# Optimization experiments

Measured on AMD Instinct MI355X. Metric: run time of the kernel, lower is better.

## Reference

```python
import jax, jax.numpy as jnp
import numpy as np

HIDDEN = 2048
N_HEADS = 32
N_KV_HEADS = 8
HEAD_DIM = 64
ROPE_THETA = 500000.0
B, S = 1, 2048


def _rope_tables(seq_len):
    inv_freq = 1.0 / ROPE_THETA ** (jnp.arange(0, HEAD_DIM, 2, dtype=jnp.float32) / HEAD_DIM)
    angles = jnp.arange(seq_len, dtype=jnp.float32)[:, None] * inv_freq[None, :]
    return jnp.cos(angles), jnp.sin(angles)


def _apply_rope(x, cos, sin):
    # x: (B, S, H, D); cos/sin: (S, D//2)
    x1 = x[..., 0::2]
    x2 = x[..., 1::2]
    c = cos[None, :, None, :]
    s = sin[None, :, None, :]
    x1r = x1 * c - x2 * s
    x2r = x1 * s + x2 * c
    return jnp.stack([x1r, x2r], axis=-1).reshape(x.shape)


def setup_inputs() -> dict:
    key = jax.random.key(0)
    ks = jax.random.split(key, 5)
    hidden_states = jax.random.normal(ks[0], (B, S, HIDDEN), dtype=jnp.float32)
    # causal mask, broadcastable over (B, H, S, S)
    attention_mask = jnp.tril(jnp.ones((S, S), dtype=bool))[None, :, :]
    sc = 1.0 / np.sqrt(HIDDEN)
    wq = jax.random.normal(ks[1], (HIDDEN, N_HEADS * HEAD_DIM), dtype=jnp.float32) * sc
    wk = jax.random.normal(ks[2], (HIDDEN, N_KV_HEADS * HEAD_DIM), dtype=jnp.float32) * sc
    wv = jax.random.normal(ks[3], (HIDDEN, N_KV_HEADS * HEAD_DIM), dtype=jnp.float32) * sc
    wo = jax.random.normal(ks[4], (N_HEADS * HEAD_DIM, HIDDEN), dtype=jnp.float32) * sc
    return {"hidden_states": hidden_states, "attention_mask": attention_mask,
            "wq": wq, "wk": wk, "wv": wv, "wo": wo}


def reference(hidden_states, attention_mask, wq, wk, wv, wo):
    b, s, _ = hidden_states.shape
    groups = N_HEADS // N_KV_HEADS
    q = (hidden_states @ wq).reshape(b, s, N_HEADS, HEAD_DIM)
    k = (hidden_states @ wk).reshape(b, s, N_KV_HEADS, HEAD_DIM)
    v = (hidden_states @ wv).reshape(b, s, N_KV_HEADS, HEAD_DIM)
    cos, sin = _rope_tables(s)
    q = _apply_rope(q, cos, sin)
    k = _apply_rope(k, cos, sin)
    k = jnp.repeat(k, groups, axis=2)  # (b, s, H, D)
    v = jnp.repeat(v, groups, axis=2)
    q = q.transpose(0, 2, 1, 3)  # (b, H, s, D)
    k = k.transpose(0, 2, 1, 3)
    v = v.transpose(0, 2, 1, 3)
    scores = jnp.einsum('bhqd,bhkd->bhqk', q, k) / jnp.sqrt(jnp.float32(HEAD_DIM))
    scores = jnp.where(attention_mask[:, None, :, :], scores, -jnp.inf)
    probs = jax.nn.softmax(scores, axis=-1)
    out = jnp.einsum('bhqk,bhkd->bhqd', probs, v)
    out = out.transpose(0, 2, 1, 3).reshape(b, s, N_HEADS * HEAD_DIM)
    return out @ wo
```

## Files before the change

kernel.cpp:

```cpp
#include <hip/hip_runtime.h>

typedef __attribute__((ext_vector_type(8))) short short8;
typedef __attribute__((ext_vector_type(4))) float float4v;

union U4S8 { uint4 u; short8 s; };

__device__ __forceinline__ float bf2f(ushort u) {
    union { uint i; float f; } v; v.i = ((uint)u) << 16; return v.f;
}
__device__ __forceinline__ ushort f2bf(float f) {
    union { uint i; float f; } v; v.f = f;
    return (ushort)((v.i + 0x7FFFu + ((v.i >> 16) & 1u)) >> 16);
}
#if __has_builtin(__builtin_amdgcn_cvt_pk_bf16_f32)
__device__ __forceinline__ uint f2bf_pk(float a, float b) {
    auto r = __builtin_amdgcn_cvt_pk_bf16_f32(a, b);
    return __builtin_bit_cast(uint, r);
}
#else
__device__ __forceinline__ uint f2bf_pk(float a, float b) {
    return (uint)f2bf(a) | ((uint)f2bf(b) << 16);
}
#endif
__device__ __forceinline__ void gld_lds16(const ushort* g, ushort* l) {
    __builtin_amdgcn_global_load_lds((const __attribute__((address_space(1))) unsigned int*)g,
                                     (__attribute__((address_space(3))) unsigned int*)l,
                                     16, 0, 0);
}

__device__ __forceinline__ void tconv_body(const float* in, ushort* out,
                                           int C, int r0, int c0, int tid) {
    __shared__ float t[64][65];
    const int lrow = tid >> 2;
    const int lc   = (tid & 3) * 16;
    const float* ip = in + (size_t)(r0 + lrow) * C + c0 + lc;
#pragma unroll
    for (int i = 0; i < 4; i++) {
        float4 v = *(const float4*)(ip + 4 * i);
        t[lrow][lc + 4 * i + 0] = v.x; t[lrow][lc + 4 * i + 1] = v.y;
        t[lrow][lc + 4 * i + 2] = v.z; t[lrow][lc + 4 * i + 3] = v.w;
    }
    __syncthreads();
    ushort* op = out + (size_t)(c0 + lrow) * 2048 + r0 + lc;
#pragma unroll
    for (int i = 0; i < 8; i++)
        ((uint*)op)[i] = f2bf_pk(t[lc + 2 * i][lrow], t[lc + 2 * i + 1][lrow]);
}

__global__ __launch_bounds__(256) void prep(const float* __restrict__ hidden,
                                            const float* __restrict__ wq,
                                            const float* __restrict__ wk,
                                            const float* __restrict__ wv,
                                            const float* __restrict__ wo,
                                            ushort* __restrict__ hid,
                                            ushort* __restrict__ wT,
                                            ushort* __restrict__ woT) {
    const int bx = blockIdx.x;
    if (bx < 2048) {
        const size_t i = ((size_t)bx * 256 + threadIdx.x) * 8;
        float4 a = *(const float4*)(hidden + i);
        float4 b = *(const float4*)(hidden + i + 4);
        uint4 u;
        u.x = f2bf_pk(a.x, a.y); u.y = f2bf_pk(a.z, a.w);
        u.z = f2bf_pk(b.x, b.y); u.w = f2bf_pk(b.z, b.w);
        *(uint4*)(hid + i) = u;
    } else if (bx < 3584) {
        const int i = bx - 2048;
        const int xx = i % 48, yy = i / 48;
        const float* in; ushort* op; int C, cx;
        if (xx < 32)      { in = wq; op = wT;                        C = 2048; cx = xx; }
        else if (xx < 40) { in = wk; op = wT + (size_t)2048 * 2048;  C = 512;  cx = xx - 32; }
        else              { in = wv; op = wT + (size_t)2560 * 2048;  C = 512;  cx = xx - 40; }
        tconv_body(in, op, C, yy * 64, cx * 64, threadIdx.x);
    } else {
        const int i = bx - 3584;
        tconv_body(wo, woT, 2048, (i >> 5) * 64, (i & 31) * 64, threadIdx.x);
    }
}

template <bool BF16OUT>
__global__ __launch_bounds__(512, 2) void gemm_n128(const ushort* __restrict__ A,
                                                    const ushort* __restrict__ Bt,
                                                    void* __restrict__ Cout,
                                                    int N, int K, int lda, int ropeQKV) {
    __shared__ ushort As[2][2][128 * 32];
    __shared__ ushort Bs[2][2][128 * 32];

    const int tid = threadIdx.x, w = tid >> 6, lane = tid & 63;
    const int lr = lane & 15, quad = lane >> 4;
    const int m0 = blockIdx.x * 128, n0 = blockIdx.y * 128;
    const int wr = w >> 1, wc = w & 1;

    const int srow = lane >> 2;
    const int skb  = (lane & 3) ^ ((srow >> 1) & 3);

    const ushort* Ap = A  + (size_t)(m0 + 16 * w + srow) * lda + skb * 8;
    const ushort* Bp = Bt + (size_t)(n0 + 16 * w + srow) * K + skb * 8;

    float4v acc[2][4];
#pragma unroll
    for (int a = 0; a < 2; a++)
#pragma unroll
        for (int b = 0; b < 4; b++) { acc[a][b][0] = 0.f; acc[a][b][1] = 0.f; acc[a][b][2] = 0.f; acc[a][b][3] = 0.f; }

    const int fsw = (lr >> 1) & 3;
    const int niter = K >> 6;

    gld_lds16(Ap,      &As[0][0][w * 512]);
    gld_lds16(Ap + 32, &As[0][1][w * 512]);
    gld_lds16(Bp,      &Bs[0][0][w * 512]);
    gld_lds16(Bp + 32, &Bs[0][1][w * 512]);

    for (int it = 0; it < niter; it++) {
        const int b = it & 1;

        asm volatile("s_waitcnt vmcnt(0) lgkmcnt(0)\n\ts_barrier" ::: "memory");

        if (it + 1 < niter) {
            const int k1 = (it + 1) << 6;
            gld_lds16(Ap + k1,      &As[1 - b][0][w * 512]);
            gld_lds16(Ap + k1 + 32, &As[1 - b][1][w * 512]);
            gld_lds16(Bp + k1,      &Bs[1 - b][0][w * 512]);
            gld_lds16(Bp + k1 + 32, &Bs[1 - b][1][w * 512]);
        }

#pragma unroll
        for (int kh = 0; kh < 2; kh++) {
            short8 af[2], bf[4];
#pragma unroll
            for (int mt = 0; mt < 2; mt++)
                af[mt] = *(const short8*)&As[b][kh][(wr * 32 + mt * 16 + lr) * 32 + (quad ^ fsw) * 8];
#pragma unroll
            for (int nt = 0; nt < 4; nt++)
                bf[nt] = *(const short8*)&Bs[b][kh][(wc * 64 + nt * 16 + lr) * 32 + (quad ^ fsw) * 8];
#pragma unroll
            for (int mt = 0; mt < 2; mt++)
#pragma unroll
                for (int nt = 0; nt < 4; nt++)
                    acc[mt][nt] = __builtin_amdgcn_mfma_f32_16x16x32_bf16(af[mt], bf[nt], acc[mt][nt], 0, 0, 0);
        }
    }

    const int rbase = m0 + wr * 32 + quad * 4;
    const int cbase = n0 + wc * 64 + lr;
    if (BF16OUT) {
        ushort* Cb = (ushort*)Cout;
        if (ropeQKV && (int)blockIdx.y < 20) {
            const float osc = ((int)blockIdx.y < 16) ? 0.18033688f : 1.0f;
            const float sgn = (lr & 1) ? 1.0f : -1.0f;
#pragma unroll
            for (int nt = 0; nt < 4; nt++) {
                const int col = cbase + nt * 16;
                const int j = (col >> 1) & 31;
                const float inv = __expf(-(float)(2 * j) * (1.0f / 64.0f) * 13.122363377404328f);
#pragma unroll
                for (int mt = 0; mt < 2; mt++)
#pragma unroll
                    for (int r = 0; r < 4; r++) {
                        const int row = rbase + mt * 16 + r;
                        float sn, cs;
                        sincosf((float)row * inv, &sn, &cs);
                        const float mine = acc[mt][nt][r];
                        const float partner = __shfl_xor(mine, 1);
                        Cb[(size_t)row * N + col] = f2bf((mine * cs + sgn * partner * sn) * osc);
                    }
            }
        } else {
#pragma unroll
            for (int mt = 0; mt < 2; mt++)
#pragma unroll
                for (int nt = 0; nt < 4; nt++)
#pragma unroll
                    for (int r = 0; r < 4; r++)
                        Cb[(size_t)(rbase + mt * 16 + r) * N + cbase + nt * 16] = f2bf(acc[mt][nt][r]);
        }
    } else {
        float* Cf = (float*)Cout;
#pragma unroll
        for (int mt = 0; mt < 2; mt++)
#pragma unroll
            for (int nt = 0; nt < 4; nt++)
#pragma unroll
                for (int r = 0; r < 4; r++)
                    Cf[(size_t)(rbase + mt * 16 + r) * N + cbase + nt * 16] = acc[mt][nt][r];
    }
}

__global__ __launch_bounds__(256) void attn_mfma(const ushort* __restrict__ Q,
                                                 const ushort* __restrict__ Kc,
                                                 const ushort* __restrict__ Vc,
                                                 ushort* __restrict__ O0,
                                                 ushort* __restrict__ O1,
                                                 float* __restrict__ L0,
                                                 float* __restrict__ L1) {
    __shared__ ushort Ks[2][64 * 64];
    __shared__ ushort Vt[2][64 * 64];
    __shared__ ushort Ps[4][16 * 64];

    const int tid = threadIdx.x, w = tid >> 6, lane = tid & 63;
    const int lr = lane & 15, quad = lane >> 4;
    const int h = blockIdx.y, g = h >> 2, z = blockIdx.z;

    const int dg = tid & 15;
    const int kl = tid >> 4;
    const int ksub = lane >> 3, dsub = lane & 7;
    ushort* Pw = Ps[w];
    ushort* Op = z ? O1 : O0;
    float*  Lp = z ? L1 : L0;

    const ushort* Vp0 = Vc + g * 64 + dg * 4 + (size_t)3072 * kl;
    const ushort* Kp0 = Kc + g * 64 + ((dsub ^ ksub) * 8) + (size_t)3072 * ksub;

    short8 onesf;
#pragma unroll
    for (int j = 0; j < 8; j++) onesf[j] = (short)0x3F80;

    for (int ti = 0; ti < 2; ti++) {
        const int bx = ti ? 31 - (int)blockIdx.x : (int)blockIdx.x;
        const int nch = (bx >= z) ? ((bx - z) >> 1) + 1 : 0;
        const int last = z + 2 * (nch - 1);

        const ushort* qp = Q + (size_t)(bx * 64 + w * 16 + lr) * 3072 + h * 64 + quad * 8;
        const short8 qf0 = *(const short8*)qp;
        const short8 qf1 = *(const short8*)(qp + 32);

        float4v oacc[4], lacc;
#pragma unroll
        for (int t = 0; t < 4; t++) { oacc[t][0] = 0.f; oacc[t][1] = 0.f; oacc[t][2] = 0.f; oacc[t][3] = 0.f; }
        lacc[0] = 0.f; lacc[1] = 0.f; lacc[2] = 0.f; lacc[3] = 0.f;

        uint2 vv[4];
        if (nch) {
#pragma unroll
            for (int t = 0; t < 4; t++)
                vv[t] = *(const uint2*)(Vp0 + (size_t)(z * 64 + 16 * t) * 3072);
        }
        __syncthreads();
        if (nch) {
#pragma unroll
            for (int i = 0; i < 2; i++) {
                const int rt = 2 * w + i;
                gld_lds16(Kp0 + (size_t)(z * 64 + rt * 8) * 3072, &Ks[0][rt * 512]);
            }
        }

        for (int c = 0; c < nch; c++) {
            const int kb = z + 2 * c;
            const int b = c & 1;
            ushort* bKs = Ks[b];
            ushort* bVt = Vt[b];

#pragma unroll
            for (int i = 0; i < 4; i++) {
                const uint sel = (i & 1) ? 0x07060302u : 0x05040100u;
                uint s0 = (i < 2) ? vv[0].x : vv[0].y;
                uint s1 = (i < 2) ? vv[1].x : vv[1].y;
                uint s2 = (i < 2) ? vv[2].x : vv[2].y;
                uint s3 = (i < 2) ? vv[3].x : vv[3].y;
                uint2 pk;
                pk.x = __builtin_amdgcn_perm(s1, s0, sel);
                pk.y = __builtin_amdgcn_perm(s3, s2, sel);
                *(uint2*)&bVt[(dg * 4 + i) * 64 + (kl ^ ((dg & 3) * 4 + i)) * 4] = pk;
            }

            const int kn = (c + 1 < nch) ? kb + 2 : last;
#pragma unroll
            for (int t = 0; t < 4; t++)
                vv[t] = *(const uint2*)(Vp0 + (size_t)(kn * 64 + 16 * t) * 3072);

            asm volatile("s_waitcnt vmcnt(4) lgkmcnt(0)\n\ts_barrier" ::: "memory");

#pragma unroll
            for (int i = 0; i < 2; i++) {
                const int rt = 2 * w + i;
                gld_lds16(Kp0 + (size_t)(kn * 64 + rt * 8) * 3072, &Ks[1 - b][rt * 512]);
            }

            float4v sacc[4];
#pragma unroll
            for (int t = 0; t < 4; t++) { sacc[t][0] = 0.f; sacc[t][1] = 0.f; sacc[t][2] = 0.f; sacc[t][3] = 0.f; }
#pragma unroll
            for (int t = 0; t < 4; t++) {
                const int krow = t * 16 + lr;
                const int sw = lr & 7;
                short8 kf0 = *(const short8*)&bKs[krow * 64 + ((quad)     ^ sw) * 8];
                short8 kf1 = *(const short8*)&bKs[krow * 64 + ((quad + 4) ^ sw) * 8];
                sacc[t] = __builtin_amdgcn_mfma_f32_16x16x32_bf16(qf0, kf0, sacc[t], 0, 0, 0);
                sacc[t] = __builtin_amdgcn_mfma_f32_16x16x32_bf16(qf1, kf1, sacc[t], 0, 0, 0);
            }

            if (kb == bx) {
#pragma unroll
                for (int r = 0; r < 4; r++) {
                    const int qr = w * 16 + quad * 4 + r;
                    float p0 = exp2f(sacc[0][r]), p1 = exp2f(sacc[1][r]);
                    float p2 = exp2f(sacc[2][r]), p3 = exp2f(sacc[3][r]);
                    if (lr > qr)      p0 = 0.f;
                    if (16 + lr > qr) p1 = 0.f;
                    if (32 + lr > qr) p2 = 0.f;
                    if (48 + lr > qr) p3 = 0.f;
                    const int prow = quad * 4 + r;
                    uint2 pk; pk.x = f2bf_pk(p0, p1); pk.y = f2bf_pk(p2, p3);
                    *(uint2*)&Pw[prow * 64 + (lr ^ prow) * 4] = pk;
                }
            } else {
#pragma unroll
                for (int r = 0; r < 4; r++) {
                    const int prow = quad * 4 + r;
                    uint2 pk;
                    pk.x = f2bf_pk(exp2f(sacc[0][r]), exp2f(sacc[1][r]));
                    pk.y = f2bf_pk(exp2f(sacc[2][r]), exp2f(sacc[3][r]));
                    *(uint2*)&Pw[prow * 64 + (lr ^ prow) * 4] = pk;
                }
            }

#pragma unroll
            for (int ks2 = 0; ks2 < 2; ks2++) {
                const int ub = ks2 * 8 + quad * 2;
                U4S8 pu;
                uint2 plo = *(const uint2*)&Pw[lr * 64 + ((ub)     ^ lr) * 4];
                uint2 phi = *(const uint2*)&Pw[lr * 64 + ((ub + 1) ^ lr) * 4];
                pu.u.x = plo.x; pu.u.y = plo.y; pu.u.z = phi.x; pu.u.w = phi.y;
                lacc = __builtin_amdgcn_mfma_f32_16x16x32_bf16(pu.s, onesf, lacc, 0, 0, 0);
#pragma unroll
                for (int t = 0; t < 4; t++) {
                    const int d = t * 16 + lr;
                    U4S8 vu;
                    uint2 vlo = *(const uint2*)&bVt[d * 64 + ((ub)     ^ lr) * 4];
                    uint2 vhi = *(const uint2*)&bVt[d * 64 + ((ub + 1) ^ lr) * 4];
                    vu.u.x = vlo.x; vu.u.y = vlo.y; vu.u.z = vhi.x; vu.u.w = vhi.y;
                    oacc[t] = __builtin_amdgcn_mfma_f32_16x16x32_bf16(pu.s, vu.s, oacc[t], 0, 0, 0);
                }
            }
        }

        ushort* op = Op + (size_t)(bx * 64 + w * 16 + quad * 4) * 2048 + h * 64 + lr;
#pragma unroll
        for (int t = 0; t < 4; t++)
#pragma unroll
            for (int r = 0; r < 4; r++)
                op[(size_t)r * 2048 + t * 16] = f2bf(oacc[t][r]);
        if (lr == 0) {
#pragma unroll
            for (int r = 0; r < 4; r++)
                Lp[h * 2048 + bx * 64 + w * 16 + quad * 4 + r] = lacc[r];
        }
    }
}

__global__ __launch_bounds__(256) void combine(ushort* __restrict__ O0,
                                               const ushort* __restrict__ O1,
                                               const float* __restrict__ L0,
                                               const float* __restrict__ L1) {
    const int idx = blockIdx.x * 256 + threadIdx.x;
    const int r = idx >> 8;
    const int c8 = (idx & 255) * 8;
    const int h = c8 >> 6;
    const float rl = 1.0f / (L0[h * 2048 + r] + L1[h * 2048 + r]);
    uint4 a = *(const uint4*)(O0 + (size_t)r * 2048 + c8);
    uint4 b = *(const uint4*)(O1 + (size_t)r * 2048 + c8);
    uint ua[4] = {a.x, a.y, a.z, a.w}, ub[4] = {b.x, b.y, b.z, b.w};
    uint rr[4];
#pragma unroll
    for (int k = 0; k < 4; k++) {
        float x0 = bf2f((ushort)(ua[k] & 0xFFFFu)) + bf2f((ushort)(ub[k] & 0xFFFFu));
        float x1 = bf2f((ushort)(ua[k] >> 16))     + bf2f((ushort)(ub[k] >> 16));
        rr[k] = f2bf_pk(x0 * rl, x1 * rl);
    }
    uint4 res; res.x = rr[0]; res.y = rr[1]; res.z = rr[2]; res.w = rr[3];
    *(uint4*)(O0 + (size_t)r * 2048 + c8) = res;
}

extern "C" void kernel_launch(void* const* d_in, const int* in_sizes, int n_in,
                              void* d_out, int out_size, void* d_ws, size_t ws_size,
                              hipStream_t stream) {
    const float* hidden = (const float*)d_in[0];
    const float* wq = (const float*)d_in[2];
    const float* wk = (const float*)d_in[3];
    const float* wv = (const float*)d_in[4];
    const float* wo = (const float*)d_in[5];

    ushort* ws = (ushort*)d_ws;
    ushort* hid = ws;
    ushort* wT  = ws + 4194304;
    ushort* woT = ws + 10485760;
    ushort* O1  = wT;
    float*  L0  = (float*)(ws + 8388608);
    float*  L1  = L0 + 65536;
    ushort* QKV = (ushort*)d_out;

    prep<<<4608, 256, 0, stream>>>(hidden, wq, wk, wv, wo, hid, wT, woT);
    gemm_n128<true><<<dim3(16, 24), 512, 0, stream>>>(hid, wT, QKV, 3072, 2048, 2048, 1);
    attn_mfma<<<dim3(16, 32, 2), 256, 0, stream>>>(QKV, QKV + 2048, QKV + 2560,
                                                   hid , O1, L0, L1);
    combine<<<2048, 256, 0, stream>>>(hid, O1, L0, L1);
    gemm_n128<false><<<dim3(16, 16), 512, 0, stream>>>(hid, woT, d_out, 2048, 2048, 2048, 0);
}
```

Measured before the change: 237.2 us.

## Write V pre-transposed from QKV GEMM epilogue and async-load it in attention

The QKV projection epilogue now writes V in a transposed, swizzled layout into a separate buffer. The attention kernel can then stream V into LDS with direct global-to-LDS copies, the same way it loads K. This removes the per-chunk register loads, byte-permute transpose and LDS stores of V inside the attention loop. In exchange the wait becomes vmcnt(0), which waits on the whole prefetch, and the GEMM epilogue does scattered 4-byte transposed stores.

Measured after the change: 233.2 us. Within noise of the previous version (-1.7%).

```diff
diff --git a/kernel.cpp b/kernel.cpp
--- a/kernel.cpp
+++ b/kernel.cpp
@@ -82,7 +82,8 @@
 __global__ __launch_bounds__(512, 2) void gemm_n128(const ushort* __restrict__ A,
                                                     const ushort* __restrict__ Bt,
                                                     void* __restrict__ Cout,
-                                                    int N, int K, int lda, int ropeQKV) {
+                                                    int N, int K, int lda, int ropeQKV,
+                                                    ushort* __restrict__ VTout) {
     __shared__ ushort As[2][2][128 * 32];
     __shared__ ushort Bs[2][2][128 * 32];
 
@@ -145,7 +146,22 @@
     const int cbase = n0 + wc * 64 + lr;
     if (BF16OUT) {
         ushort* Cb = (ushort*)Cout;
-        if (ropeQKV && (int)blockIdx.y < 20) {
+        if (ropeQKV && (int)blockIdx.y >= 20) {
+            const int ch = rbase >> 6;
+            const int j2 = (wr & 1) * 2;
+#pragma unroll
+            for (int nt = 0; nt < 4; nt++) {
+                const int vd = cbase + nt * 16 - 2560;
+                const int vx = vd & 15;
+#pragma unroll
+                for (int r = 0; r < 4; r++) {
+                    const int kl = quad * 4 + r;
+                    const uint pk = f2bf_pk(acc[0][nt][r], acc[1][nt][r]);
+                    *(uint*)(VTout + (size_t)vd * 2048 + ch * 64
+                             + ((kl ^ vx) << 2) + j2) = pk;
+                }
+            }
+        } else if (ropeQKV && (int)blockIdx.y < 20) {
             const float osc = ((int)blockIdx.y < 16) ? 0.18033688f : 1.0f;
             const float sgn = (lr & 1) ? 1.0f : -1.0f;
 #pragma unroll
@@ -188,7 +204,7 @@
 
 __global__ __launch_bounds__(256) void attn_mfma(const ushort* __restrict__ Q,
                                                  const ushort* __restrict__ Kc,
-                                                 const ushort* __restrict__ Vc,
+                                                 const ushort* __restrict__ VT,
                                                  ushort* __restrict__ O0,
                                                  ushort* __restrict__ O1,
                                                  float* __restrict__ L0,
@@ -201,15 +217,13 @@
     const int lr = lane & 15, quad = lane >> 4;
     const int h = blockIdx.y, g = h >> 2, z = blockIdx.z;
 
-    const int dg = tid & 15;
-    const int kl = tid >> 4;
     const int ksub = lane >> 3, dsub = lane & 7;
     ushort* Pw = Ps[w];
     ushort* Op = z ? O1 : O0;
     float*  Lp = z ? L1 : L0;
 
-    const ushort* Vp0 = Vc + g * 64 + dg * 4 + (size_t)3072 * kl;
     const ushort* Kp0 = Kc + g * 64 + ((dsub ^ ksub) * 8) + (size_t)3072 * ksub;
+    const ushort* Vp0 = VT + (size_t)(g * 64 + ksub) * 2048 + dsub * 8;
 
     short8 onesf;
 #pragma unroll
@@ -218,7 +232,6 @@
     for (int ti = 0; ti < 2; ti++) {
         const int bx = ti ? 31 - (int)blockIdx.x : (int)blockIdx.x;
         const int nch = (bx >= z) ? ((bx - z) >> 1) + 1 : 0;
-        const int last = z + 2 * (nch - 1);
 
         const ushort* qp = Q + (size_t)(bx * 64 + w * 16 + lr) * 3072 + h * 64 + quad * 8;
         const short8 qf0 = *(const short8*)qp;
@@ -229,18 +242,13 @@
         for (int t = 0; t < 4; t++) { oacc[t][0] = 0.f; oacc[t][1] = 0.f; oacc[t][2] = 0.f; oacc[t][3] = 0.f; }
         lacc[0] = 0.f; lacc[1] = 0.f; lacc[2] = 0.f; lacc[3] = 0.f;
 
-        uint2 vv[4];
-        if (nch) {
-#pragma unroll
-            for (int t = 0; t < 4; t++)
-                vv[t] = *(const uint2*)(Vp0 + (size_t)(z * 64 + 16 * t) * 3072);
-        }
         __syncthreads();
         if (nch) {
 #pragma unroll
             for (int i = 0; i < 2; i++) {
                 const int rt = 2 * w + i;
                 gld_lds16(Kp0 + (size_t)(z * 64 + rt * 8) * 3072, &Ks[0][rt * 512]);
+                gld_lds16(Vp0 + (size_t)(rt * 8) * 2048 + z * 64, &Vt[0][rt * 512]);
             }
         }
 
@@ -250,30 +258,16 @@
             ushort* bKs = Ks[b];
             ushort* bVt = Vt[b];
 
-#pragma unroll
-            for (int i = 0; i < 4; i++) {
-                const uint sel = (i & 1) ? 0x07060302u : 0x05040100u;
-                uint s0 = (i < 2) ? vv[0].x : vv[0].y;
-                uint s1 = (i < 2) ? vv[1].x : vv[1].y;
-                uint s2 = (i < 2) ? vv[2].x : vv[2].y;
-                uint s3 = (i < 2) ? vv[3].x : vv[3].y;
-                uint2 pk;
-                pk.x = __builtin_amdgcn_perm(s1, s0, sel);
-                pk.y = __builtin_amdgcn_perm(s3, s2, sel);
-                *(uint2*)&bVt[(dg * 4 + i) * 64 + (kl ^ ((dg & 3) * 4 + i)) * 4] = pk;
-            }
-
-            const int kn = (c + 1 < nch) ? kb + 2 : last;
-#pragma unroll
-            for (int t = 0; t < 4; t++)
-                vv[t] = *(const uint2*)(Vp0 + (size_t)(kn * 64 + 16 * t) * 3072);
-
-            asm volatile("s_waitcnt vmcnt(4) lgkmcnt(0)\n\ts_barrier" ::: "memory");
-
-#pragma unroll
-            for (int i = 0; i < 2; i++) {
-                const int rt = 2 * w + i;
-                gld_lds16(Kp0 + (size_t)(kn * 64 + rt * 8) * 3072, &Ks[1 - b][rt * 512]);
+            asm volatile("s_waitcnt vmcnt(0) lgkmcnt(0)\n\ts_barrier" ::: "memory");
+
+            if (c + 1 < nch) {
+                const int kn = kb + 2;
+#pragma unroll
+                for (int i = 0; i < 2; i++) {
+                    const int rt = 2 * w + i;
+                    gld_lds16(Kp0 + (size_t)(kn * 64 + rt * 8) * 3072, &Ks[1 - b][rt * 512]);
+                    gld_lds16(Vp0 + (size_t)(rt * 8) * 2048 + kn * 64, &Vt[1 - b][rt * 512]);
+                }
             }
 
             float4v sacc[4];
@@ -388,11 +382,12 @@
     float*  L0  = (float*)(ws + 8388608);
     float*  L1  = L0 + 65536;
     ushort* QKV = (ushort*)d_out;
+    ushort* VT  = QKV + 6291456;
 
     prep<<<4608, 256, 0, stream>>>(hidden, wq, wk, wv, wo, hid, wT, woT);
-    gemm_n128<true><<<dim3(16, 24), 512, 0, stream>>>(hid, wT, QKV, 3072, 2048, 2048, 1);
-    attn_mfma<<<dim3(16, 32, 2), 256, 0, stream>>>(QKV, QKV + 2048, QKV + 2560,
+    gemm_n128<true><<<dim3(16, 24), 512, 0, stream>>>(hid, wT, QKV, 3072, 2048, 2048, 1, VT);
+    attn_mfma<<<dim3(16, 32, 2), 256, 0, stream>>>(QKV, QKV + 2048, VT,
                                                    hid , O1, L0, L1);
     combine<<<2048, 256, 0, stream>>>(hid, O1, L0, L1);
-    gemm_n128<false><<<dim3(16, 16), 512, 0, stream>>>(hid, woT, d_out, 2048, 2048, 2048, 0);
-}
+    gemm_n128<false><<<dim3(16, 16), 512, 0, stream>>>(hid, woT, d_out, 2048, 2048, 2048, 0, nullptr);
+}
```
